# Kernel optimization log

Measured on AMD Instinct MI355X. Metric: run time of the kernel, lower is better.

Reference implementation:

```python
import jax, jax.numpy as jnp
import numpy as np

N_EMBD = 1024
N_HEAD = 16
HEAD_DIM = N_EMBD // N_HEAD


def setup_inputs() -> dict:
    key = jax.random.key(0)
    k1, k2, k3 = jax.random.split(key, 3)
    x = jax.random.normal(k1, (2, 2048, N_EMBD), dtype=jnp.float32)
    # torch Linear weight shapes: c_attn [3*n_embd, n_embd], c_proj [n_embd, n_embd]
    w_attn = jax.random.normal(k2, (3 * N_EMBD, N_EMBD), dtype=jnp.float32) * 0.02
    w_proj = jax.random.normal(k3, (N_EMBD, N_EMBD), dtype=jnp.float32) * 0.02
    return {"x": x, "w_attn": w_attn, "w_proj": w_proj}


def reference(x, w_attn, w_proj):
    B, T, C = x.shape
    qkv = x @ w_attn.T  # [B,T,3C]
    q, k, v = jnp.split(qkv, 3, axis=2)
    # [B,T,H,D] -> [B,H,T,D]
    def heads(t):
        return t.reshape(B, T, N_HEAD, HEAD_DIM).transpose(0, 2, 1, 3)
    q, k, v = heads(q), heads(k), heads(v)
    scale = 1.0 / jnp.sqrt(jnp.asarray(HEAD_DIM, dtype=x.dtype))
    att = jnp.einsum('bhqd,bhkd->bhqk', q, k) * scale
    causal = jnp.tril(jnp.ones((T, T), dtype=bool))
    att = jnp.where(causal[None, None], att, jnp.asarray(-jnp.inf, dtype=att.dtype))
    att = jax.nn.softmax(att, axis=-1)
    y = jnp.einsum('bhqk,bhkd->bhqd', att, v)
    y = y.transpose(0, 2, 1, 3).reshape(B, T, C)
    return y @ w_proj.T
```

## Files before the change

kernel.cpp:

```cpp
#include <hip/hip_runtime.h>

#define BSZ 2
#define SEQ 2048
#define NEMBD 1024
#define NHEAD 16
#define HDIM 64
#define BT (BSZ * SEQ)
#define QKV_LD (3 * NEMBD)
#define SCALE_LOG2E 0.1803368665f

typedef unsigned short u16;
typedef __attribute__((ext_vector_type(8))) short short8;
typedef __attribute__((ext_vector_type(4))) float floatx4;
typedef __attribute__((ext_vector_type(4))) unsigned short ushort4v;

#define MFMA16(a, b, c) __builtin_amdgcn_mfma_f32_16x16x32_bf16(a, b, c, 0, 0, 0)

__device__ __forceinline__ void gload_lds16(const void* g, void* l) {
  __builtin_amdgcn_global_load_lds(
      (const __attribute__((address_space(1))) unsigned int*)(g),
      (__attribute__((address_space(3))) unsigned int*)(l), 16, 0, 0);
}

__device__ __forceinline__ u16 f2bf(float f) {
  unsigned int u = __builtin_bit_cast(unsigned int, f);
  u += 0x7FFFu + ((u >> 16) & 1u);
  return (u16)(u >> 16);
}

__global__ __launch_bounds__(256) void cvt_bf16(const float* __restrict__ in,
                                                u16* __restrict__ out, int n) {
  int i = (blockIdx.x * 256 + threadIdx.x) * 8;
  if (i >= n) return;
  float4 a = *(const float4*)(in + i);
  float4 b = *(const float4*)(in + i + 4);
  short8 o;
  o[0] = (short)f2bf(a.x); o[1] = (short)f2bf(a.y);
  o[2] = (short)f2bf(a.z); o[3] = (short)f2bf(a.w);
  o[4] = (short)f2bf(b.x); o[5] = (short)f2bf(b.y);
  o[6] = (short)f2bf(b.z); o[7] = (short)f2bf(b.w);
  *(short8*)(out + i) = o;
}

__global__ __launch_bounds__(256) void gemm_qkv(const u16* __restrict__ A,
                                                const u16* __restrict__ B,
                                                u16* __restrict__ qkb,
                                                u16* __restrict__ vtg) {
  __shared__ __align__(16) u16 As[128 * 32];
  __shared__ __align__(16) u16 Bs[128 * 32];
  const int t = threadIdx.x;
  const int lane = t & 63, w = t >> 6;
  const int l15 = lane & 15, quad = lane >> 4;
  const int wm = w >> 1, wn = w & 1;
  const int m0 = blockIdx.y * 128, n0 = blockIdx.x * 128;

  const int srow = t >> 2;
  const int scol = (t & 3) * 8;
  const u16* ga = A + (size_t)(m0 + srow) * NEMBD + scol;
  const u16* gb = B + (size_t)(n0 + srow) * NEMBD + scol;

  floatx4 acc[4][4] = {};

  for (int k0 = 0; k0 < NEMBD; k0 += 32) {
    __syncthreads();
    gload_lds16(ga + k0, &As[t * 8]);
    gload_lds16(ga + (size_t)64 * NEMBD + k0, &As[2048 + t * 8]);
    gload_lds16(gb + k0, &Bs[t * 8]);
    gload_lds16(gb + (size_t)64 * NEMBD + k0, &Bs[2048 + t * 8]);
    __syncthreads();
    short8 af[4], bfr[4];
#pragma unroll
    for (int mt = 0; mt < 4; ++mt)
      af[mt] = *(const short8*)&As[(wm * 64 + mt * 16 + l15) * 32 + quad * 8];
#pragma unroll
    for (int nt = 0; nt < 4; ++nt)
      bfr[nt] = *(const short8*)&Bs[(wn * 64 + nt * 16 + l15) * 32 + quad * 8];
#pragma unroll
    for (int mt = 0; mt < 4; ++mt)
#pragma unroll
      for (int nt = 0; nt < 4; ++nt)
        acc[mt][nt] = MFMA16(af[mt], bfr[nt], acc[mt][nt]);
  }

  if (n0 >= 2 * NEMBD) {
#pragma unroll
    for (int mt = 0; mt < 4; ++mt)
#pragma unroll
      for (int nt = 0; nt < 4; ++nt) {
        int hd = n0 + wn * 64 + nt * 16 + l15 - 2 * NEMBD;
        int token = m0 + wm * 64 + mt * 16 + quad * 4;
        int b = token >> 11, tp = token & (SEQ - 1);
        ushort4v pk;
#pragma unroll
        for (int r = 0; r < 4; ++r) pk[r] = f2bf(acc[mt][nt][r]);
        *(ushort4v*)&vtg[((size_t)(b * NEMBD + hd)) * SEQ + tp] = pk;
      }
  } else {
#pragma unroll
    for (int mt = 0; mt < 4; ++mt)
#pragma unroll
      for (int nt = 0; nt < 4; ++nt)
#pragma unroll
        for (int r = 0; r < 4; ++r) {
          size_t row = (size_t)(m0 + wm * 64 + mt * 16 + quad * 4 + r);
          size_t col = (size_t)(n0 + wn * 64 + nt * 16 + l15);
          qkb[row * 2048 + col] = f2bf(acc[mt][nt][r]);
        }
  }
}

__global__ __launch_bounds__(256) void attn_mfma3(const u16* __restrict__ qkb,
                                                  const u16* __restrict__ vtg,
                                                  u16* __restrict__ opart,
                                                  float* __restrict__ lpart) {
  const int bx = blockIdx.x;
  const int qt = 15 - (bx >> 6);
  const int r6 = bx & 63;
  const int bh = r6 >> 1, half = r6 & 1;
  const int b = bh >> 4, h = bh & 15;
  const int t = threadIdx.x, lane = t & 63, w = t >> 6;
  const int l15 = lane & 15, quad = lane >> 4;

  __shared__ __align__(16) u16 Qs[128 * 64];
  __shared__ __align__(16) u16 Ks[64 * 64];
  __shared__ __align__(16) u16 Vt[64 * 64];
  __shared__ __align__(16) u16 Pa[128 * 72];

  {
    const u16* qb = qkb + ((size_t)(b * SEQ + qt * 128)) * 2048 + h * HDIM;
#pragma unroll
    for (int is = 0; is < 4; ++is) {
      int s = is * 256 + t;
      int row = s >> 3, pos = s & 7;
      int kc = pos ^ (row & 7);
      gload_lds16(qb + (size_t)row * 2048 + kc * 8, &Qs[s * 8]);
    }
  }
  __syncthreads();
  short8 qf[2][2];
#pragma unroll
  for (int qs = 0; qs < 2; ++qs) {
    int qrow = w * 32 + qs * 16 + l15;
#pragma unroll
    for (int hf = 0; hf < 2; ++hf)
      qf[qs][hf] = *(const short8*)&Qs[qrow * 64 + (((hf * 4 + quad) ^ (qrow & 7)) * 8)];
  }

  float rs[2] = {0.f, 0.f};
  floatx4 o_acc[2][4] = {};

  const int kt0 = half ? (qt + 1) : 0;
  const int kt_end = kt0 + qt + 1;
  const int um_end = (kt_end < 2 * qt) ? kt_end : (2 * qt);

#define ATTN_TILE(KT, MASKED)                                                  \
  {                                                                            \
    __syncthreads();                                                           \
    const u16* kb = qkb + ((size_t)(b * SEQ + (KT) * 64)) * 2048 + NEMBD + h * HDIM; \
    const u16* vb = vtg + ((size_t)(bh * 64)) * SEQ + (KT) * 64;               \
    _Pragma("unroll")                                                          \
    for (int is = 0; is < 2; ++is) {                                           \
      int s = is * 256 + t;                                                    \
      int row = s >> 3, pos = s & 7;                                           \
      int kc = pos ^ (row & 7);                                                \
      gload_lds16(kb + (size_t)row * 2048 + kc * 8, &Ks[s * 8]);               \
      gload_lds16(vb + (size_t)row * SEQ + kc * 8, &Vt[s * 8]);                \
    }                                                                          \
    __syncthreads();                                                           \
    floatx4 sacc[2][4];                                                        \
    _Pragma("unroll")                                                          \
    for (int nt = 0; nt < 4; ++nt) {                                           \
      int krow = nt * 16 + l15;                                                \
      short8 kf0 = *(const short8*)&Ks[krow * 64 + ((quad ^ (krow & 7)) * 8)]; \
      short8 kf1 = *(const short8*)&Ks[krow * 64 + (((4 + quad) ^ (krow & 7)) * 8)]; \
      _Pragma("unroll")                                                        \
      for (int qs = 0; qs < 2; ++qs) {                                         \
        floatx4 z = {0.f, 0.f, 0.f, 0.f};                                      \
        z = MFMA16(kf0, qf[qs][0], z);                                         \
        z = MFMA16(kf1, qf[qs][1], z);                                         \
        sacc[qs][nt] = z;                                                      \
      }                                                                        \
    }                                                                          \
    _Pragma("unroll")                                                          \
    for (int qs = 0; qs < 2; ++qs) {                                           \
      const int qg = qt * 128 + w * 32 + qs * 16 + l15;                        \
      const int kb0 = (KT) * 64 + quad * 4;                                    \
      _Pragma("unroll")                                                        \
      for (int nt = 0; nt < 4; ++nt) {                                         \
        ushort4v pk;                                                           \
        _Pragma("unroll")                                                      \
        for (int r = 0; r < 4; ++r) {                                          \
          float p = exp2f(fmaf(sacc[qs][nt][r], SCALE_LOG2E, -8.0f));          \
          if (MASKED && (kb0 + nt * 16 + r) > qg) p = 0.0f;                    \
          rs[qs] += p;                                                         \
          pk[r] = f2bf(p);                                                     \
        }                                                                      \
        *(ushort4v*)&Pa[(w * 32 + qs * 16 + l15) * 72 + nt * 16 + quad * 4] = pk; \
      }                                                                        \
    }                                                                          \
    short8 pf[2][2];                                                           \
    _Pragma("unroll")                                                          \
    for (int qs = 0; qs < 2; ++qs) {                                           \
      const int prow = w * 32 + qs * 16 + l15;                                 \
      pf[qs][0] = *(const short8*)&Pa[prow * 72 + quad * 8];                   \
      pf[qs][1] = *(const short8*)&Pa[prow * 72 + 32 + quad * 8];              \
    }                                                                          \
    _Pragma("unroll")                                                          \
    for (int nt = 0; nt < 4; ++nt) {                                           \
      int drow = nt * 16 + l15;                                                \
      short8 vf0 = *(const short8*)&Vt[drow * 64 + ((quad ^ (drow & 7)) * 8)]; \
      short8 vf1 = *(const short8*)&Vt[drow * 64 + (((4 + quad) ^ (drow & 7)) * 8)]; \
      _Pragma("unroll")                                                        \
      for (int qs = 0; qs < 2; ++qs) {                                         \
        o_acc[qs][nt] = MFMA16(pf[qs][0], vf0, o_acc[qs][nt]);                 \
        o_acc[qs][nt] = MFMA16(pf[qs][1], vf1, o_acc[qs][nt]);                 \
      }                                                                        \
    }                                                                          \
  }

  int kt = kt0;
  for (; kt < um_end; ++kt) ATTN_TILE(kt, 0);
  for (; kt < kt_end; ++kt) ATTN_TILE(kt, 1);
#undef ATTN_TILE

#pragma unroll
  for (int qs = 0; qs < 2; ++qs) {
    rs[qs] += __shfl_xor(rs[qs], 16, 64);
    rs[qs] += __shfl_xor(rs[qs], 32, 64);
    if (quad == 0)
      lpart[((size_t)half * 32 + bh) * SEQ + qt * 128 + w * 32 + qs * 16 + l15] = rs[qs];
  }
  u16* ob = opart + (size_t)half * BT * NEMBD;
#pragma unroll
  for (int qs = 0; qs < 2; ++qs)
#pragma unroll
    for (int nt = 0; nt < 4; ++nt)
#pragma unroll
      for (int r = 0; r < 4; ++r) {
        size_t tok = (size_t)(b * SEQ + qt * 128 + w * 32 + qs * 16 + quad * 4 + r);
        ob[tok * NEMBD + h * HDIM + nt * 16 + l15] = f2bf(o_acc[qs][nt][r]);
      }
}

__global__ __launch_bounds__(256) void combine(const u16* __restrict__ opart,
                                               const float* __restrict__ lpart,
                                               u16* __restrict__ yb) {
  int idx = (blockIdx.x * 256 + threadIdx.x) * 4;
  int tok = idx >> 10, c = idx & 1023;
  int b = tok >> 11, q = tok & (SEQ - 1), h = c >> 6;
  float l = lpart[(size_t)(b * 16 + h) * SEQ + q] +
            lpart[(size_t)(32 + b * 16 + h) * SEQ + q];
  float inv = 1.0f / l;
  ushort4v o0 = *(const ushort4v*)&opart[idx];
  ushort4v o1 = *(const ushort4v*)&opart[(size_t)BT * NEMBD + idx];
  ushort4v yo;
#pragma unroll
  for (int j = 0; j < 4; ++j) {
    float f0 = __builtin_bit_cast(float, (unsigned)o0[j] << 16);
    float f1 = __builtin_bit_cast(float, (unsigned)o1[j] << 16);
    yo[j] = f2bf((f0 + f1) * inv);
  }
  *(ushort4v*)&yb[idx] = yo;
}

__global__ __launch_bounds__(256) void gemm_out(const u16* __restrict__ A,
                                                const u16* __restrict__ B,
                                                float* __restrict__ C) {
  __shared__ __align__(16) u16 As[128 * 32];
  __shared__ __align__(16) u16 Bs[64 * 32];
  const int t = threadIdx.x;
  const int lane = t & 63, w = t >> 6;
  const int l15 = lane & 15, quad = lane >> 4;
  const int wm = w >> 1, wn = w & 1;
  const int m0 = blockIdx.y * 128, n0 = blockIdx.x * 64;

  const int srow = t >> 2;
  const int scol = (t & 3) * 8;
  const u16* ga = A + (size_t)(m0 + srow) * NEMBD + scol;
  const u16* gb = B + (size_t)(n0 + srow) * NEMBD + scol;

  floatx4 acc[4][2] = {};

  for (int k0 = 0; k0 < NEMBD; k0 += 32) {
    __syncthreads();
    gload_lds16(ga + k0, &As[t * 8]);
    gload_lds16(ga + (size_t)64 * NEMBD + k0, &As[2048 + t * 8]);
    gload_lds16(gb + k0, &Bs[t * 8]);
    __syncthreads();
    short8 af[4], bfr[2];
#pragma unroll
    for (int mt = 0; mt < 4; ++mt)
      af[mt] = *(const short8*)&As[(wm * 64 + mt * 16 + l15) * 32 + quad * 8];
#pragma unroll
    for (int nt = 0; nt < 2; ++nt)
      bfr[nt] = *(const short8*)&Bs[(wn * 32 + nt * 16 + l15) * 32 + quad * 8];
#pragma unroll
    for (int mt = 0; mt < 4; ++mt)
#pragma unroll
      for (int nt = 0; nt < 2; ++nt)
        acc[mt][nt] = MFMA16(af[mt], bfr[nt], acc[mt][nt]);
  }

#pragma unroll
  for (int mt = 0; mt < 4; ++mt)
#pragma unroll
    for (int nt = 0; nt < 2; ++nt)
#pragma unroll
      for (int r = 0; r < 4; ++r) {
        size_t row = (size_t)(m0 + wm * 64 + mt * 16 + quad * 4 + r);
        size_t col = (size_t)(n0 + wn * 32 + nt * 16 + l15);
        C[row * NEMBD + col] = acc[mt][nt][r];
      }
}

extern "C" void kernel_launch(void* const* d_in, const int* in_sizes, int n_in,
                              void* d_out, int out_size, void* d_ws, size_t ws_size,
                              hipStream_t stream) {
  const float* x      = (const float*)d_in[0];
  const float* w_attn = (const float*)d_in[1];
  const float* w_proj = (const float*)d_in[2];
  float* out = (float*)d_out;

  u16* base  = (u16*)d_ws;
  u16* opart = base;
  u16* xb    = base;
  u16* wab   = base + 4194304;
  u16* wpb   = base + 8388608;
  u16* qkb   = base + 9437184;
  u16* vtg   = base + 17825792;
  u16* yb    = base + 22020096;
  float* lpart = (float*)(base + 26214400);

  cvt_bf16<<<(BT * NEMBD) / 2048, 256, 0, stream>>>(x, xb, BT * NEMBD);
  cvt_bf16<<<(QKV_LD * NEMBD) / 2048, 256, 0, stream>>>(w_attn, wab, QKV_LD * NEMBD);
  cvt_bf16<<<(NEMBD * NEMBD) / 2048, 256, 0, stream>>>(w_proj, wpb, NEMBD * NEMBD);

  gemm_qkv<<<dim3(QKV_LD / 128, BT / 128), 256, 0, stream>>>(xb, wab, qkb, vtg);

  attn_mfma3<<<dim3((SEQ / 128) * BSZ * NHEAD * 2), 256, 0, stream>>>(qkb, vtg, opart, lpart);

  combine<<<(BT * NEMBD) / 1024, 256, 0, stream>>>(opart, lpart, yb);

  gemm_out<<<dim3(NEMBD / 64, BT / 128), 256, 0, stream>>>(yb, wpb, out);
}
```

Measured before the change: 205.0 us.

## Merge input conversions, deepen GEMM K tiles with XOR-swizzled LDS, vectorize epilogues

```diff
diff --git a/kernel.cpp b/kernel.cpp
--- a/kernel.cpp
+++ b/kernel.cpp
@@ -28,61 +28,87 @@
   return (u16)(u >> 16);
 }
 
-__global__ __launch_bounds__(256) void cvt_bf16(const float* __restrict__ in,
-                                                u16* __restrict__ out, int n) {
+#define N_X  (BT * NEMBD)
+#define N_WA (QKV_LD * NEMBD)
+#define N_WP (NEMBD * NEMBD)
+__global__ __launch_bounds__(256) void cvt_all(const float* __restrict__ x,
+                                               const float* __restrict__ wa,
+                                               const float* __restrict__ wp,
+                                               u16* __restrict__ xb,
+                                               u16* __restrict__ wab,
+                                               u16* __restrict__ wpb) {
   int i = (blockIdx.x * 256 + threadIdx.x) * 8;
-  if (i >= n) return;
-  float4 a = *(const float4*)(in + i);
-  float4 b = *(const float4*)(in + i + 4);
+  const float* src;
+  u16* dst;
+  if (i < N_X)            { src = x + i;              dst = xb + i; }
+  else if (i < N_X + N_WA){ src = wa + (i - N_X);     dst = wab + (i - N_X); }
+  else                    { src = wp + (i - N_X - N_WA); dst = wpb + (i - N_X - N_WA); }
+  float4 a = *(const float4*)(src);
+  float4 b = *(const float4*)(src + 4);
   short8 o;
   o[0] = (short)f2bf(a.x); o[1] = (short)f2bf(a.y);
   o[2] = (short)f2bf(a.z); o[3] = (short)f2bf(a.w);
   o[4] = (short)f2bf(b.x); o[5] = (short)f2bf(b.y);
   o[6] = (short)f2bf(b.z); o[7] = (short)f2bf(b.w);
-  *(short8*)(out + i) = o;
+  *(short8*)(dst) = o;
 }
 
 __global__ __launch_bounds__(256) void gemm_qkv(const u16* __restrict__ A,
                                                 const u16* __restrict__ B,
                                                 u16* __restrict__ qkb,
                                                 u16* __restrict__ vtg) {
-  __shared__ __align__(16) u16 As[128 * 32];
-  __shared__ __align__(16) u16 Bs[128 * 32];
+  __shared__ __align__(16) u16 As[128 * 64];
+  __shared__ __align__(16) u16 Bs[128 * 64];
   const int t = threadIdx.x;
   const int lane = t & 63, w = t >> 6;
   const int l15 = lane & 15, quad = lane >> 4;
   const int wm = w >> 1, wn = w & 1;
   const int m0 = blockIdx.y * 128, n0 = blockIdx.x * 128;
-
-  const int srow = t >> 2;
-  const int scol = (t & 3) * 8;
-  const u16* ga = A + (size_t)(m0 + srow) * NEMBD + scol;
-  const u16* gb = B + (size_t)(n0 + srow) * NEMBD + scol;
+  const int is_v = (n0 >= 2 * NEMBD);
 
   floatx4 acc[4][4] = {};
 
-  for (int k0 = 0; k0 < NEMBD; k0 += 32) {
+  for (int k0 = 0; k0 < NEMBD; k0 += 64) {
     __syncthreads();
-    gload_lds16(ga + k0, &As[t * 8]);
-    gload_lds16(ga + (size_t)64 * NEMBD + k0, &As[2048 + t * 8]);
-    gload_lds16(gb + k0, &Bs[t * 8]);
-    gload_lds16(gb + (size_t)64 * NEMBD + k0, &Bs[2048 + t * 8]);
+#pragma unroll
+    for (int is = 0; is < 4; ++is) {
+      int s = is * 256 + t;
+      int row = s >> 3, pos = s & 7;
+      int kc = pos ^ (row & 7);
+      gload_lds16(A + (size_t)(m0 + row) * NEMBD + k0 + kc * 8, &As[s * 8]);
+      gload_lds16(B + (size_t)(n0 + row) * NEMBD + k0 + kc * 8, &Bs[s * 8]);
+    }
     __syncthreads();
-    short8 af[4], bfr[4];
-#pragma unroll
-    for (int mt = 0; mt < 4; ++mt)
-      af[mt] = *(const short8*)&As[(wm * 64 + mt * 16 + l15) * 32 + quad * 8];
-#pragma unroll
-    for (int nt = 0; nt < 4; ++nt)
-      bfr[nt] = *(const short8*)&Bs[(wn * 64 + nt * 16 + l15) * 32 + quad * 8];
-#pragma unroll
-    for (int mt = 0; mt < 4; ++mt)
-#pragma unroll
-      for (int nt = 0; nt < 4; ++nt)
-        acc[mt][nt] = MFMA16(af[mt], bfr[nt], acc[mt][nt]);
-  }
-
-  if (n0 >= 2 * NEMBD) {
+#pragma unroll
+    for (int kh = 0; kh < 2; ++kh) {
+      short8 af[4], bfr[4];
+#pragma unroll
+      for (int mt = 0; mt < 4; ++mt) {
+        int row = wm * 64 + mt * 16 + l15;
+        af[mt] = *(const short8*)&As[row * 64 + (((kh * 4 + quad) ^ (row & 7)) * 8)];
+      }
+#pragma unroll
+      for (int nt = 0; nt < 4; ++nt) {
+        int row = wn * 64 + nt * 16 + l15;
+        bfr[nt] = *(const short8*)&Bs[row * 64 + (((kh * 4 + quad) ^ (row & 7)) * 8)];
+      }
+      if (is_v) {
+#pragma unroll
+        for (int mt = 0; mt < 4; ++mt)
+#pragma unroll
+          for (int nt = 0; nt < 4; ++nt)
+            acc[mt][nt] = MFMA16(af[mt], bfr[nt], acc[mt][nt]);
+      } else {
+#pragma unroll
+        for (int mt = 0; mt < 4; ++mt)
+#pragma unroll
+          for (int nt = 0; nt < 4; ++nt)
+            acc[mt][nt] = MFMA16(bfr[nt], af[mt], acc[mt][nt]);
+      }
+    }
+  }
+
+  if (is_v) {
 #pragma unroll
     for (int mt = 0; mt < 4; ++mt)
 #pragma unroll
@@ -97,15 +123,17 @@
       }
   } else {
 #pragma unroll
-    for (int mt = 0; mt < 4; ++mt)
-#pragma unroll
-      for (int nt = 0; nt < 4; ++nt)
-#pragma unroll
-        for (int r = 0; r < 4; ++r) {
-          size_t row = (size_t)(m0 + wm * 64 + mt * 16 + quad * 4 + r);
-          size_t col = (size_t)(n0 + wn * 64 + nt * 16 + l15);
-          qkb[row * 2048 + col] = f2bf(acc[mt][nt][r]);
-        }
+    for (int mt = 0; mt < 4; ++mt) {
+      size_t token = (size_t)(m0 + wm * 64 + mt * 16 + l15);
+#pragma unroll
+      for (int nt = 0; nt < 4; ++nt) {
+        int nc = n0 + wn * 64 + nt * 16 + quad * 4;
+        ushort4v pk;
+#pragma unroll
+        for (int r = 0; r < 4; ++r) pk[r] = f2bf(acc[mt][nt][r]);
+        *(ushort4v*)&qkb[token * 2048 + nc] = pk;
+      }
+    }
   }
 }
 
@@ -266,51 +294,65 @@
 __global__ __launch_bounds__(256) void gemm_out(const u16* __restrict__ A,
                                                 const u16* __restrict__ B,
                                                 float* __restrict__ C) {
-  __shared__ __align__(16) u16 As[128 * 32];
-  __shared__ __align__(16) u16 Bs[64 * 32];
+  __shared__ __align__(16) u16 As[128 * 64];
+  __shared__ __align__(16) u16 Bs[64 * 64];
   const int t = threadIdx.x;
   const int lane = t & 63, w = t >> 6;
   const int l15 = lane & 15, quad = lane >> 4;
   const int wm = w >> 1, wn = w & 1;
   const int m0 = blockIdx.y * 128, n0 = blockIdx.x * 64;
 
-  const int srow = t >> 2;
-  const int scol = (t & 3) * 8;
-  const u16* ga = A + (size_t)(m0 + srow) * NEMBD + scol;
-  const u16* gb = B + (size_t)(n0 + srow) * NEMBD + scol;
-
   floatx4 acc[4][2] = {};
 
-  for (int k0 = 0; k0 < NEMBD; k0 += 32) {
+  for (int k0 = 0; k0 < NEMBD; k0 += 64) {
     __syncthreads();
-    gload_lds16(ga + k0, &As[t * 8]);
-    gload_lds16(ga + (size_t)64 * NEMBD + k0, &As[2048 + t * 8]);
-    gload_lds16(gb + k0, &Bs[t * 8]);
+#pragma unroll
+    for (int is = 0; is < 4; ++is) {
+      int s = is * 256 + t;
+      int row = s >> 3, pos = s & 7;
+      int kc = pos ^ (row & 7);
+      gload_lds16(A + (size_t)(m0 + row) * NEMBD + k0 + kc * 8, &As[s * 8]);
+    }
+#pragma unroll
+    for (int is = 0; is < 2; ++is) {
+      int s = is * 256 + t;
+      int row = s >> 3, pos = s & 7;
+      int kc = pos ^ (row & 7);
+      gload_lds16(B + (size_t)(n0 + row) * NEMBD + k0 + kc * 8, &Bs[s * 8]);
+    }
     __syncthreads();
-    short8 af[4], bfr[2];
-#pragma unroll
-    for (int mt = 0; mt < 4; ++mt)
-      af[mt] = *(const short8*)&As[(wm * 64 + mt * 16 + l15) * 32 + quad * 8];
-#pragma unroll
-    for (int nt = 0; nt < 2; ++nt)
-      bfr[nt] = *(const short8*)&Bs[(wn * 32 + nt * 16 + l15) * 32 + quad * 8];
-#pragma unroll
-    for (int mt = 0; mt < 4; ++mt)
-#pragma unroll
-      for (int nt = 0; nt < 2; ++nt)
-        acc[mt][nt] = MFMA16(af[mt], bfr[nt], acc[mt][nt]);
-  }
-
-#pragma unroll
-  for (int mt = 0; mt < 4; ++mt)
-#pragma unroll
-    for (int nt = 0; nt < 2; ++nt)
-#pragma unroll
-      for (int r = 0; r < 4; ++r) {
-        size_t row = (size_t)(m0 + wm * 64 + mt * 16 + quad * 4 + r);
-        size_t col = (size_t)(n0 + wn * 32 + nt * 16 + l15);
-        C[row * NEMBD + col] = acc[mt][nt][r];
-      }
+#pragma unroll
+    for (int kh = 0; kh < 2; ++kh) {
+      short8 af[4], bfr[2];
+#pragma unroll
+      for (int mt = 0; mt < 4; ++mt) {
+        int row = wm * 64 + mt * 16 + l15;
+        af[mt] = *(const short8*)&As[row * 64 + (((kh * 4 + quad) ^ (row & 7)) * 8)];
+      }
+#pragma unroll
+      for (int nt = 0; nt < 2; ++nt) {
+        int row = wn * 32 + nt * 16 + l15;
+        bfr[nt] = *(const short8*)&Bs[row * 64 + (((kh * 4 + quad) ^ (row & 7)) * 8)];
+      }
+#pragma unroll
+      for (int mt = 0; mt < 4; ++mt)
+#pragma unroll
+        for (int nt = 0; nt < 2; ++nt)
+          acc[mt][nt] = MFMA16(bfr[nt], af[mt], acc[mt][nt]);
+    }
+  }
+
+#pragma unroll
+  for (int mt = 0; mt < 4; ++mt) {
+    size_t token = (size_t)(m0 + wm * 64 + mt * 16 + l15);
+#pragma unroll
+    for (int nt = 0; nt < 2; ++nt) {
+      int nc = n0 + wn * 32 + nt * 16 + quad * 4;
+      float4 v = make_float4(acc[mt][nt][0], acc[mt][nt][1],
+                             acc[mt][nt][2], acc[mt][nt][3]);
+      *(float4*)&C[token * NEMBD + nc] = v;
+    }
+  }
 }
 
 extern "C" void kernel_launch(void* const* d_in, const int* in_sizes, int n_in,
@@ -331,9 +373,7 @@
   u16* yb    = base + 22020096;
   float* lpart = (float*)(base + 26214400);
 
-  cvt_bf16<<<(BT * NEMBD) / 2048, 256, 0, stream>>>(x, xb, BT * NEMBD);
-  cvt_bf16<<<(QKV_LD * NEMBD) / 2048, 256, 0, stream>>>(w_attn, wab, QKV_LD * NEMBD);
-  cvt_bf16<<<(NEMBD * NEMBD) / 2048, 256, 0, stream>>>(w_proj, wpb, NEMBD * NEMBD);
+  cvt_all<<<(N_X + N_WA + N_WP) / 2048, 256, 0, stream>>>(x, w_attn, w_proj, xb, wab, wpb);
 
   gemm_qkv<<<dim3(QKV_LD / 128, BT / 128), 256, 0, stream>>>(xb, wab, qkb, vtg);
 
```

New measurement: 204.5 us. About the same (-0.2%).
